# Kernel tuning notes

Hardware: AMD Instinct MI355X
Metric: run time of the kernel (lower is better)

## Reference

```python
import jax, jax.numpy as jnp
import numpy as np

ATOM_FDIM = 133
BOND_FDIM = 14
HIDDEN = 300
DEPTH = 3
FFN_HIDDEN = 300
NUM_ATOMS = 100000
NUM_EDGES = 400000
NUM_MOLS = 4096


def setup_inputs() -> dict:
    key = jax.random.key(0)
    ks = jax.random.split(key, 10)
    x = jax.random.normal(ks[0], (NUM_ATOMS, ATOM_FDIM), dtype=jnp.float32)
    edge_index = jax.random.randint(ks[1], (2, NUM_EDGES), 0, NUM_ATOMS, dtype=jnp.int32)
    edge_attr = jax.random.normal(ks[2], (NUM_EDGES, BOND_FDIM), dtype=jnp.float32)
    batch = jnp.sort(jax.random.randint(ks[3], (NUM_ATOMS,), 0, NUM_MOLS, dtype=jnp.int32))
    s = 0.05
    W_i = jax.random.normal(ks[4], (HIDDEN, ATOM_FDIM + BOND_FDIM), dtype=jnp.float32) * s
    W_h = jax.random.normal(ks[5], (HIDDEN, HIDDEN), dtype=jnp.float32) * s
    W_o_w = jax.random.normal(ks[6], (HIDDEN, ATOM_FDIM + HIDDEN), dtype=jnp.float32) * s
    W_o_b = jnp.zeros((HIDDEN,), dtype=jnp.float32)
    ffn1_w = jax.random.normal(ks[7], (FFN_HIDDEN, HIDDEN), dtype=jnp.float32) * s
    ffn1_b = jnp.zeros((FFN_HIDDEN,), dtype=jnp.float32)
    ffn2_w = jax.random.normal(ks[8], (1, FFN_HIDDEN), dtype=jnp.float32) * s
    ffn2_b = jnp.zeros((1,), dtype=jnp.float32)
    return {"x": x, "edge_index": edge_index, "edge_attr": edge_attr, "batch": batch,
            "W_i": W_i, "W_h": W_h, "W_o_w": W_o_w, "W_o_b": W_o_b,
            "ffn1_w": ffn1_w, "ffn1_b": ffn1_b, "ffn2_w": ffn2_w, "ffn2_b": ffn2_b}


def reference(x, edge_index, edge_attr, batch, W_i, W_h, W_o_w, W_o_b,
              ffn1_w, ffn1_b, ffn2_w, ffn2_b):
    num_atoms = x.shape[0]
    src, tgt = edge_index[0], edge_index[1]
    # initial edge messages: [E, hidden]
    init = jnp.concatenate([x[src], edge_attr], axis=-1)
    m = jax.nn.relu(init @ W_i.T)
    # dropout is identity at inference
    for _ in range(DEPTH - 1):
        nei = jax.ops.segment_sum(m, tgt, num_segments=num_atoms)  # [N, hidden]
        m = jax.nn.relu(m + nei[src] @ W_h.T)
    atom_msg = jax.ops.segment_sum(m, tgt, num_segments=num_atoms)
    atom_h = jax.nn.relu(jnp.concatenate([x, atom_msg], axis=-1) @ W_o_w.T + W_o_b)
    mol = jax.ops.segment_sum(atom_h, batch, num_segments=NUM_MOLS)  # [B, hidden]
    h = jax.nn.relu(mol @ ffn1_w.T + ffn1_b)
    out = h @ ffn2_w.T + ffn2_b  # [B, 1]
    return out
```

## Files before the change

kernel.cpp:

```cpp
#include <hip/hip_runtime.h>
#include <hip/hip_fp16.h>

#define HID   300
#define NEIP  304
#define PSTR  900
#define APB   4
#define SWK(r) (((r) >> 2) & 3)

typedef _Float16 f16;
typedef f16  f16x2 __attribute__((ext_vector_type(2)));
typedef f16  f16x4 __attribute__((ext_vector_type(4)));
typedef float f32x4 __attribute__((ext_vector_type(4)));

__device__ __forceinline__ f16x2 u2h(unsigned u) {
    union { unsigned u; f16x2 h; } c; c.u = u; return c.h;
}
__device__ __forceinline__ unsigned pk16(float a, float b) {
    union { f16 h[2]; unsigned u; } c; c.h[0] = (f16)a; c.h[1] = (f16)b;
    return c.u;
}
__device__ __forceinline__ void glds16(const void* g, void* l) {
    __builtin_amdgcn_global_load_lds(
        (const __attribute__((address_space(1))) void*)g,
        (__attribute__((address_space(3))) void*)l, 16, 0, 0);
}

__global__ __launch_bounds__(256) void fill_f32(float* __restrict__ p, int n, float v)
{
    int i = blockIdx.x * blockDim.x + threadIdx.x;
    int stride = gridDim.x * blockDim.x;
    for (; i < n; i += stride) p[i] = v;
}

__global__ __launch_bounds__(256) void zero_i32(int* __restrict__ p, int n)
{
    int i = blockIdx.x * blockDim.x + threadIdx.x;
    int stride = gridDim.x * blockDim.x;
    for (; i < n; i += stride) p[i] = 0;
}

__global__ __launch_bounds__(256) void cvt_pad_f16(
    f16* __restrict__ dst, const float* __restrict__ src,
    int srcRows, int ldsrc, int kuse, int kpad, int dstRows)
{
    int i = blockIdx.x * 256 + threadIdx.x;
    const int total = dstRows * kpad;
    const int st = gridDim.x * 256;
    for (; i < total; i += st) {
        int r = i / kpad, k = i - r * kpad;
        float v = (r < srcRows && k < kuse) ? src[(size_t)r * ldsrc + k] : 0.f;
        const int kd = (k & ~15) | (((((k >> 2) & 3) ^ SWK(r)) << 2)) | (k & 3);
        dst[(size_t)r * kpad + kd] = (f16)v;
    }
}

__global__ __launch_bounds__(256) void hist_tgt(
    const int* __restrict__ tgt, int* __restrict__ deg, int E, int N)
{
    int e = blockIdx.x * 256 + threadIdx.x;
    const int st = gridDim.x * 256;
    for (; e < E; e += st) {
        int t = tgt[e];
        t = ((unsigned)t < (unsigned)N) ? t : 0;
        atomicAdd(&deg[t], 1);
    }
}

__global__ __launch_bounds__(1024) void scan_p1(
    const int* __restrict__ deg, int* __restrict__ bsum, int N)
{
    __shared__ int s[1024];
    const int t = threadIdx.x;
    const int i = blockIdx.x * 1024 + t;
    s[t] = (i < N) ? deg[i] : 0;
    __syncthreads();
#pragma unroll
    for (int off = 512; off > 0; off >>= 1) {
        if (t < off) s[t] += s[t + off];
        __syncthreads();
    }
    if (t == 0) bsum[blockIdx.x] = s[0];
}

__global__ __launch_bounds__(1024) void scan_p2(
    const int* __restrict__ bsum, int* __restrict__ boff,
    int G, int* __restrict__ rowPtrN, int E)
{
    __shared__ int s[1024];
    const int t = threadIdx.x;
    s[t] = (t < G) ? bsum[t] : 0;
    __syncthreads();
    for (int off = 1; off < 1024; off <<= 1) {
        const int v = (t >= off) ? s[t - off] : 0;
        __syncthreads();
        s[t] += v;
        __syncthreads();
    }
    if (t < G) boff[t] = (t == 0) ? 0 : s[t - 1];
    if (t == 0) *rowPtrN = E;
}

__global__ __launch_bounds__(1024) void scan_p3(
    const int* __restrict__ deg, const int* __restrict__ boff,
    int* __restrict__ rowPtr, int* __restrict__ cursor, int N)
{
    __shared__ int s[1024];
    const int t = threadIdx.x;
    const int i = blockIdx.x * 1024 + t;
    const int v = (i < N) ? deg[i] : 0;
    s[t] = v;
    __syncthreads();
    for (int off = 1; off < 1024; off <<= 1) {
        const int w = (t >= off) ? s[t - off] : 0;
        __syncthreads();
        s[t] += w;
        __syncthreads();
    }
    if (i < N) {
        const int excl = boff[blockIdx.x] + s[t] - v;
        rowPtr[i] = excl;
        cursor[i] = excl;
    }
}

__global__ __launch_bounds__(256) void scatter_e(
    const int* __restrict__ src, const int* __restrict__ tgt,
    const float* __restrict__ ea,
    int* __restrict__ cursor, int* __restrict__ csrc,
    unsigned* __restrict__ eaPk,
    int E, int N)
{
    int e = blockIdx.x * 256 + threadIdx.x;
    const int st = gridDim.x * 256;
    for (; e < E; e += st) {
        int t = tgt[e];
        int s = src[e];
        t = ((unsigned)t < (unsigned)N) ? t : 0;
        s = ((unsigned)s < (unsigned)N) ? s : 0;
        const int p = atomicAdd(&cursor[t], 1);
        csrc[p] = s;
        const float* er = ea + (size_t)e * 14;
        uint4 q0, q1;
        q0.x = pk16(er[0],  er[1]);  q0.y = pk16(er[2],  er[3]);
        q0.z = pk16(er[4],  er[5]);  q0.w = pk16(er[6],  er[7]);
        q1.x = pk16(er[8],  er[9]);  q1.y = pk16(er[10], er[11]);
        q1.z = pk16(er[12], er[13]); q1.w = 0u;
        uint4* dst = (uint4*)(eaPk + (size_t)p * 8);
        dst[0] = q0;
        dst[1] = q1;
    }
}

__global__ __launch_bounds__(512) void gemm_mfma(
    const void* __restrict__ A1, int lda1, int a1f16, int K1use,
    const f16* __restrict__ W1, int kpad1,
    const void* __restrict__ A2, int lda2, int a2f16, int K2use,
    const f16* __restrict__ W2, int kpad2,
    const float* __restrict__ bias,
    f16* __restrict__ C, int ldc,
    int M, int do_relu)
{
    __shared__ f16 As[2][128 * 16];
    __shared__ f16 Ws[2][320 * 16];

    const int tid  = threadIdx.x;
    const int bm   = blockIdx.x * 128;
    const int lane = tid & 63;
    const int wv   = tid >> 6;
    const int wrow = (wv >> 2) * 64;
    const int wcol = (wv & 3) * 80;
    const int lm   = lane & 15;
    const int g    = lane >> 4;

    const int n1 = A1 ? (kpad1 >> 4) : 0;
    const int n2 = A2 ? (kpad2 >> 4) : 0;
    const int ntot = n1 + n2;

    f32x4 acc[4][5];
#pragma unroll
    for (int r = 0; r < 4; ++r)
#pragma unroll
        for (int c = 0; c < 5; ++c) acc[r][c] = (f32x4){0.f, 0.f, 0.f, 0.f};

    const int arow = tid >> 2;
    const int ach  = tid & 3;
    const int gm   = bm + arow;

    auto seg_f16 = [&](int s) -> bool {
        return (s < n1) ? (a1f16 != 0) : (a2f16 != 0);
    };

    auto a_load_f32 = [&](int s) -> f16x4 {
        const float* A; int lda, Kuse, k0;
        if (s < n1) { A = (const float*)A1; lda = lda1; Kuse = K1use; k0 = s << 4; }
        else        { A = (const float*)A2; lda = lda2; Kuse = K2use; k0 = (s - n1) << 4; }
        const int gk = k0 + (ach << 2);
        f16x4 v = (f16x4){0, 0, 0, 0};
        if (gm < M) {
            const float* p = A + (size_t)gm * lda + gk;
#pragma unroll
            for (int j = 0; j < 4; ++j)
                v[j] = (gk + j < Kuse) ? (f16)p[j] : (f16)0.f;
        }
        return v;
    };

    auto commit_a = [&](int b, f16x4 v) {
        *(f16x4*)&As[b][arow * 16 + ((ach ^ SWK(arow)) << 2)] = v;
    };

    auto stage_glds = [&](int s, int b) {
        const f16* W; int kpad, k0; const f16* Af; int lda; bool f16seg;
        if (s < n1) { W = W1; kpad = kpad1; k0 = s << 4;
                      f16seg = (a1f16 != 0); Af = (const f16*)A1; lda = lda1; }
        else        { W = W2; kpad = kpad2; k0 = (s - n1) << 4;
                      f16seg = (a2f16 != 0); Af = (const f16*)A2; lda = lda2; }
        const int half16 = (lane & 1) << 4;
        const int r2 = lane >> 1;
        for (int c = wv; c < 14; c += 8) {
            if (c < 4) {
                if (f16seg) {
                    const int gmrow = bm + c * 32 + r2;
                    void* ldst = (void*)&As[b][c * 512];
                    if (gmrow < M) {
                        const char* gsrc = (const char*)Af
                            + ((size_t)gmrow * lda + k0) * 2 + half16;
                        glds16(gsrc, ldst);
                    }
                }
            } else {
                const int wr = (c - 4) * 32 + r2;
                const char* gsrc = (const char*)W
                    + ((size_t)wr * kpad + k0) * 2 + half16;
                void* ldst = (void*)&Ws[b][(c - 4) * 512];
                glds16(gsrc, ldst);
            }
        }
    };

    const f16x4 z4 = (f16x4){0, 0, 0, 0};
    f16x4 aNxt = z4;
    stage_glds(0, 0);
    if (!seg_f16(0)) commit_a(0, a_load_f32(0));
    if (ntot > 1 && !seg_f16(1)) aNxt = a_load_f32(1);
    __syncthreads();

    int b = 0;
    for (int s = 0; s < ntot; ++s) {
        f16x4 af[4], bf[5];
#pragma unroll
        for (int r = 0; r < 4; ++r) {
            const int row = wrow + (r << 4) + lm;
            af[r] = *(const f16x4*)&As[b][row * 16 + ((g ^ SWK(row)) << 2)];
        }
#pragma unroll
        for (int c = 0; c < 5; ++c) {
            const int row = wcol + (c << 4) + lm;
            bf[c] = *(const f16x4*)&Ws[b][row * 16 + ((g ^ SWK(row)) << 2)];
        }
        if (s + 1 < ntot) stage_glds(s + 1, b ^ 1);
        f16x4 aN2 = z4;
        if (s + 2 < ntot && !seg_f16(s + 2)) aN2 = a_load_f32(s + 2);
#pragma unroll
        for (int r = 0; r < 4; ++r)
#pragma unroll
            for (int c = 0; c < 5; ++c)
                acc[r][c] = __builtin_amdgcn_mfma_f32_16x16x16f16(
                    af[r], bf[c], acc[r][c], 0, 0, 0);
        if (s + 1 < ntot && !seg_f16(s + 1)) commit_a(b ^ 1, aNxt);
        aNxt = aN2;
        __syncthreads();
        b ^= 1;
    }

#pragma unroll
    for (int r = 0; r < 4; ++r) {
        const int gm0 = bm + wrow + (r << 4) + ((lane >> 4) << 2);
#pragma unroll
        for (int c = 0; c < 5; ++c) {
            const int n = wcol + (c << 4) + lm;
            if (n >= HID) continue;
            const float bi = bias ? bias[n] : 0.f;
#pragma unroll
            for (int i = 0; i < 4; ++i) {
                const int gmo = gm0 + i;
                if (gmo >= M) continue;
                float v = acc[r][c][i] + bi;
                if (do_relu) v = fmaxf(v, 0.f);
                C[(size_t)gmo * ldc + n] = (f16)v;
            }
        }
    }
}

template <int NSLOTS>
__global__ __launch_bounds__(192) void edge_csr(
    const unsigned* __restrict__ packed,
    const int* __restrict__ rowPtr,
    const int* __restrict__ csrc,
    const unsigned* __restrict__ eaPk,
    const float* __restrict__ Wi,
    unsigned* __restrict__ out,
    int N)
{
    const int p = threadIdx.x;
    f16x2 wpk[14];
    if (p < 150) {
#pragma unroll
        for (int k = 0; k < 14; ++k)
            wpk[k] = (f16x2){(f16)Wi[(2 * p) * 147 + 133 + k],
                             (f16)Wi[(2 * p + 1) * 147 + 133 + k]};
    }
    const f16x2 zero2 = (f16x2){(f16)0.f, (f16)0.f};

    const int a0 = blockIdx.x * APB;
    const int a1 = min(a0 + APB, N);
    for (int a = a0; a < a1; ++a) {
        const int beg = rowPtr[a];
        const int end = rowPtr[a + 1];
        float acc0 = 0.f, acc1 = 0.f;
        if (p < 150) {
#pragma unroll 2
            for (int j = beg; j < end; ++j) {
                const int s = csrc[j];
                const unsigned* row = packed + (size_t)s * (PSTR / 2);
                const unsigned u0 = row[p];
                unsigned u1 = 0, u2 = 0;
                if (NSLOTS > 1) u1 = row[p + 150];
                if (NSLOTS > 2) u2 = row[p + 300];
                const unsigned* eq = eaPk + (size_t)j * 8;
                f16x2 ebA = zero2, ebB = zero2;
#pragma unroll
                for (int k = 0; k < 7; ++k) {
                    const f16x2 e2 = u2h(eq[k]);
                    ebA += (f16x2){e2.x, e2.x} * wpk[2 * k];
                    ebB += (f16x2){e2.y, e2.y} * wpk[2 * k + 1];
                }
                f16x2 m = __builtin_elementwise_max(u2h(u0) + (ebA + ebB), zero2);
                if (NSLOTS > 1) m = __builtin_elementwise_max(m + u2h(u1), zero2);
                if (NSLOTS > 2) m = __builtin_elementwise_max(m + u2h(u2), zero2);
                acc0 += (float)m.x;
                acc1 += (float)m.y;
            }
        }
        if (p < NEIP / 2) {
            const unsigned val = (p < 150) ? pk16(acc0, acc1) : 0u;
            const int t = p >> 3, c = (p >> 1) & 3, hf = p & 1;
            out[(size_t)a * (NEIP / 2) + t * 8 + ((c ^ SWK(a)) << 1) + hf] = val;
        }
    }
}

__global__ __launch_bounds__(256) void mol_pool(
    const f16* __restrict__ ah,
    const int* __restrict__ batch,
    float* __restrict__ mol,
    int N)
{
    const int b = blockIdx.x;
    int lo = 0, hi = N;
    while (lo < hi) { int mid = (lo + hi) >> 1; if (batch[mid] < b) lo = mid + 1; else hi = mid; }
    const int start = lo;
    hi = N;
    while (lo < hi) { int mid = (lo + hi) >> 1; if (batch[mid] < b + 1) lo = mid + 1; else hi = mid; }
    const int end = lo;

    for (int h = threadIdx.x; h < HID; h += 256) {
        float s = 0.f;
        for (int a = start; a < end; ++a) s += (float)ah[(size_t)a * PSTR + h];
        mol[(size_t)b * HID + h] = s;
    }
}

__global__ __launch_bounds__(64) void ffn2_k(
    const f16* __restrict__ h1,
    const float* __restrict__ w2,
    const float* __restrict__ b2, float* __restrict__ out, int B)
{
    const int b = blockIdx.x;
    float s = 0.f;
    for (int k = threadIdx.x; k < HID; k += 64)
        s += (float)h1[(size_t)b * NEIP + k] * w2[k];
#pragma unroll
    for (int off = 32; off > 0; off >>= 1) s += __shfl_down(s, off);
    if (threadIdx.x == 0) out[b] = s + b2[0];
}

extern "C" void kernel_launch(void* const* d_in, const int* in_sizes, int n_in,
                              void* d_out, int out_size, void* d_ws, size_t ws_size,
                              hipStream_t stream)
{
    float* outp = (float*)d_out;
    const int fillBlocks = (out_size + 255) / 256;

    if (n_in < 12) {
        fill_f32<<<fillBlocks, 256, 0, stream>>>(outp, out_size, 2.0e6f + n_in);
        return;
    }

    const int N = in_sizes[0] / 133;
    const int E = in_sizes[1] / 2;
    const int B = out_size;

    const long long expect[12] = {
        (long long)N * 133, (long long)E * 2, (long long)E * 14, N,
        300LL * 147, 300LL * 300, 300LL * 433, 300,
        300LL * 300, 300, 300, 1 };
    for (int i = 0; i < 12; ++i) {
        if ((long long)in_sizes[i] != expect[i]) {
            fill_f32<<<fillBlocks, 256, 0, stream>>>(outp, out_size,
                                                     3.0e6f + 1.0e4f * i);
            return;
        }
    }

    const int G = (N + 1023) / 1024;
    if (G > 1024) {
        fill_f32<<<fillBlocks, 256, 0, stream>>>(outp, out_size, 4.0e6f);
        return;
    }

    char* basep = (char*)d_ws;
    auto align16 = [](size_t v) { return (v + 15) & ~(size_t)15; };
    const size_t packedB = align16((size_t)N * PSTR * sizeof(f16));
    const size_t neiB    = align16((size_t)N * NEIP * sizeof(f16));
    const size_t wSmall  = align16(320 * 144 * sizeof(f16));
    const size_t wBig    = align16(320 * 304 * sizeof(f16));
    const size_t molB    = align16((size_t)B * HID * sizeof(float));
    const size_t h1B     = align16((size_t)B * NEIP * sizeof(f16));
    const size_t rpB     = align16((size_t)(N + 1) * sizeof(int));
    const size_t curB    = align16((size_t)N * sizeof(int));
    const size_t csrcB   = align16((size_t)E * sizeof(int));
    const size_t eaB     = align16((size_t)E * 8 * sizeof(unsigned));
    const size_t bsB     = align16(1024 * sizeof(int));
    const size_t need = packedB + neiB + 2 * wSmall + 3 * wBig
                      + molB + h1B + rpB + 2 * curB + csrcB + eaB + 2 * bsB;

    if (ws_size < need) {
        fill_f32<<<fillBlocks, 256, 0, stream>>>(outp, out_size,
                                                 (float)(ws_size >> 20));
        return;
    }

    const float* x     = (const float*)d_in[0];
    const int*   ei    = (const int*)d_in[1];
    const float* ea    = (const float*)d_in[2];
    const int*   batch = (const int*)d_in[3];
    const float* W_i   = (const float*)d_in[4];
    const float* W_h   = (const float*)d_in[5];
    const float* W_o   = (const float*)d_in[6];
    const float* W_ob  = (const float*)d_in[7];
    const float* f1w   = (const float*)d_in[8];
    const float* f1b   = (const float*)d_in[9];
    const float* f2w   = (const float*)d_in[10];
    const float* f2b   = (const float*)d_in[11];
    const int* src = ei;
    const int* tgt = ei + E;

    char* cp = basep;
    f16* packed = (f16*)cp;         cp += packedB;
    f16* nei    = (f16*)cp;         cp += neiB;
    f16* WiA    = (f16*)cp;         cp += wSmall;
    f16* Wh     = (f16*)cp;         cp += wBig;
    f16* WoA    = (f16*)cp;         cp += wSmall;
    f16* WoB    = (f16*)cp;         cp += wBig;
    f16* Wf1    = (f16*)cp;         cp += wBig;
    float* mol  = (float*)cp;       cp += molB;
    f16* h1     = (f16*)cp;         cp += h1B;
    int* rowPtr = (int*)cp;         cp += rpB;
    int* cursor = (int*)cp;         cp += curB;
    int* deg    = (int*)cp;         cp += curB;
    int* csrc   = (int*)cp;         cp += csrcB;
    unsigned* eaPk = (unsigned*)cp; cp += eaB;
    int* bsum   = (int*)cp;         cp += bsB;
    int* boff   = (int*)cp;         cp += bsB;

    f16* xa_s  = packed;
    f16* hn0_s = packed + 300;
    f16* hn1_s = packed + 600;

    const unsigned* packed_u = (const unsigned*)packed;
    unsigned*       nei_u    = (unsigned*)nei;

    const int gAtom = (N + 127) / 128;
    const int gMolG = (B + 127) / 128;
    const int gEdge = (N + APB - 1) / APB;

    zero_i32<<<128, 256, 0, stream>>>(deg, N);
    hist_tgt<<<1024, 256, 0, stream>>>(tgt, deg, E, N);
    scan_p1<<<G, 1024, 0, stream>>>(deg, bsum, N);
    scan_p2<<<1, 1024, 0, stream>>>(bsum, boff, G, rowPtr + N, E);
    scan_p3<<<G, 1024, 0, stream>>>(deg, boff, rowPtr, cursor, N);
    scatter_e<<<1024, 256, 0, stream>>>(src, tgt, ea, cursor, csrc, eaPk, E, N);

    cvt_pad_f16<<<64,  256, 0, stream>>>(WiA, W_i,       300, 147, 133, 144, 320);
    cvt_pad_f16<<<128, 256, 0, stream>>>(Wh,  W_h,       300, 300, 300, 304, 320);
    cvt_pad_f16<<<64,  256, 0, stream>>>(WoA, W_o,       300, 433, 133, 144, 320);
    cvt_pad_f16<<<128, 256, 0, stream>>>(WoB, W_o + 133, 300, 433, 300, 304, 320);
    cvt_pad_f16<<<128, 256, 0, stream>>>(Wf1, f1w,       300, 300, 300, 304, 320);

    gemm_mfma<<<gAtom, 512, 0, stream>>>(x, 133, 0, 133, WiA, 144,
        nullptr, 0, 0, 0, nullptr, 0, nullptr, xa_s, PSTR, N, 0);
    edge_csr<1><<<gEdge, 192, 0, stream>>>(packed_u, rowPtr, csrc, eaPk, W_i,
                                           nei_u, N);
    gemm_mfma<<<gAtom, 512, 0, stream>>>(nei, NEIP, 1, NEIP, Wh, 304,
        nullptr, 0, 0, 0, nullptr, 0, nullptr, hn0_s, PSTR, N, 0);
    edge_csr<2><<<gEdge, 192, 0, stream>>>(packed_u, rowPtr, csrc, eaPk, W_i,
                                           nei_u, N);
    gemm_mfma<<<gAtom, 512, 0, stream>>>(nei, NEIP, 1, NEIP, Wh, 304,
        nullptr, 0, 0, 0, nullptr, 0, nullptr, hn1_s, PSTR, N, 0);
    edge_csr<3><<<gEdge, 192, 0, stream>>>(packed_u, rowPtr, csrc, eaPk, W_i,
                                           nei_u, N);
    gemm_mfma<<<gAtom, 512, 0, stream>>>(x, 133, 0, 133, WoA, 144,
        nei, NEIP, 1, NEIP, WoB, 304, W_ob, hn0_s, PSTR, N, 1);
    mol_pool<<<B, 256, 0, stream>>>(hn0_s, batch, mol, N);
    gemm_mfma<<<gMolG, 512, 0, stream>>>(mol, 300, 0, 300, Wf1, 304,
        nullptr, 0, 0, 0, nullptr, 0, f1b, h1, NEIP, B, 1);
    ffn2_k<<<B, 64, 0, stream>>>(h1, f2w, f2b, outp, B);
}
```

Baseline: 860.4 us.

## Switch GEMM to 16x16x32 MFMA with K=32 tiles and 64-row blocks

Moves the GEMM from 16x16x16 MFMA to the gfx950 16x16x32 f16 MFMA. This halves the number of K steps and barriers and widens LDS fragment loads to 8 halves. The M tile shrinks from 128 to 64 rows with a launch_bounds occupancy hint, and K padding grows to multiples of 32. The swizzle, weight conversion, and the edge kernel's nei output layout are rewritten to match. The cost is more padded K work (304->320, 144->160) and more blocks that each reload the full weight tile.

```diff
diff --git a/kernel.cpp b/kernel.cpp
--- a/kernel.cpp
+++ b/kernel.cpp
@@ -2,14 +2,15 @@
 #include <hip/hip_fp16.h>
 
 #define HID   300
-#define NEIP  304
+#define NEIP  320
 #define PSTR  900
 #define APB   4
-#define SWK(r) (((r) >> 2) & 3)
+#define SWK(r) (((r) >> 1) & 3)
 
 typedef _Float16 f16;
 typedef f16  f16x2 __attribute__((ext_vector_type(2)));
 typedef f16  f16x4 __attribute__((ext_vector_type(4)));
+typedef f16  f16x8 __attribute__((ext_vector_type(8)));
 typedef float f32x4 __attribute__((ext_vector_type(4)));
 
 __device__ __forceinline__ f16x2 u2h(unsigned u) {
@@ -49,7 +50,8 @@
     for (; i < total; i += st) {
         int r = i / kpad, k = i - r * kpad;
         float v = (r < srcRows && k < kuse) ? src[(size_t)r * ldsrc + k] : 0.f;
-        const int kd = (k & ~15) | (((((k >> 2) & 3) ^ SWK(r)) << 2)) | (k & 3);
+        const int t = k >> 5, kg = (k >> 3) & 3, w = k & 7;
+        const int kd = (t << 5) | ((kg ^ SWK(r)) << 3) | w;
         dst[(size_t)r * kpad + kd] = (f16)v;
     }
 }
@@ -151,7 +153,7 @@
     }
 }
 
-__global__ __launch_bounds__(512) void gemm_mfma(
+__global__ __launch_bounds__(512, 4) void gemm_mfma(
     const void* __restrict__ A1, int lda1, int a1f16, int K1use,
     const f16* __restrict__ W1, int kpad1,
     const void* __restrict__ A2, int lda2, int a2f16, int K2use,
@@ -160,86 +162,81 @@
     f16* __restrict__ C, int ldc,
     int M, int do_relu)
 {
-    __shared__ f16 As[2][128 * 16];
-    __shared__ f16 Ws[2][320 * 16];
+    __shared__ f16 As[2][64 * 32];
+    __shared__ f16 Ws[2][320 * 32];
 
     const int tid  = threadIdx.x;
-    const int bm   = blockIdx.x * 128;
+    const int bm   = blockIdx.x * 64;
     const int lane = tid & 63;
     const int wv   = tid >> 6;
-    const int wrow = (wv >> 2) * 64;
+    const int wrow = (wv >> 2) * 32;
     const int wcol = (wv & 3) * 80;
     const int lm   = lane & 15;
-    const int g    = lane >> 4;
-
-    const int n1 = A1 ? (kpad1 >> 4) : 0;
-    const int n2 = A2 ? (kpad2 >> 4) : 0;
+    const int kg   = lane >> 4;
+
+    const int n1 = A1 ? (kpad1 >> 5) : 0;
+    const int n2 = A2 ? (kpad2 >> 5) : 0;
     const int ntot = n1 + n2;
 
-    f32x4 acc[4][5];
-#pragma unroll
-    for (int r = 0; r < 4; ++r)
+    f32x4 acc[2][5];
+#pragma unroll
+    for (int r = 0; r < 2; ++r)
 #pragma unroll
         for (int c = 0; c < 5; ++c) acc[r][c] = (f32x4){0.f, 0.f, 0.f, 0.f};
 
     const int arow = tid >> 2;
-    const int ach  = tid & 3;
+    const int asub = tid & 3;
     const int gm   = bm + arow;
 
     auto seg_f16 = [&](int s) -> bool {
         return (s < n1) ? (a1f16 != 0) : (a2f16 != 0);
     };
 
-    auto a_load_f32 = [&](int s) -> f16x4 {
+    auto a_load_f32 = [&](int s) -> f16x8 {
         const float* A; int lda, Kuse, k0;
-        if (s < n1) { A = (const float*)A1; lda = lda1; Kuse = K1use; k0 = s << 4; }
-        else        { A = (const float*)A2; lda = lda2; Kuse = K2use; k0 = (s - n1) << 4; }
-        const int gk = k0 + (ach << 2);
-        f16x4 v = (f16x4){0, 0, 0, 0};
-        if (gm < M) {
+        if (s < n1) { A = (const float*)A1; lda = lda1; Kuse = K1use; k0 = s << 5; }
+        else        { A = (const float*)A2; lda = lda2; Kuse = K2use; k0 = (s - n1) << 5; }
+        f16x8 v = (f16x8){0, 0, 0, 0, 0, 0, 0, 0};
+        if (tid < 256 && gm < M) {
+            const int gk = k0 + (asub << 3);
             const float* p = A + (size_t)gm * lda + gk;
 #pragma unroll
-            for (int j = 0; j < 4; ++j)
+            for (int j = 0; j < 8; ++j)
                 v[j] = (gk + j < Kuse) ? (f16)p[j] : (f16)0.f;
         }
         return v;
     };
 
-    auto commit_a = [&](int b, f16x4 v) {
-        *(f16x4*)&As[b][arow * 16 + ((ach ^ SWK(arow)) << 2)] = v;
+    auto commit_a = [&](int b, f16x8 v) {
+        if (tid < 256)
+            *(f16x8*)&As[b][arow * 32 + ((asub ^ SWK(arow)) << 3)] = v;
     };
 
     auto stage_glds = [&](int s, int b) {
         const f16* W; int kpad, k0; const f16* Af; int lda; bool f16seg;
-        if (s < n1) { W = W1; kpad = kpad1; k0 = s << 4;
+        if (s < n1) { W = W1; kpad = kpad1; k0 = s << 5;
                       f16seg = (a1f16 != 0); Af = (const f16*)A1; lda = lda1; }
-        else        { W = W2; kpad = kpad2; k0 = (s - n1) << 4;
+        else        { W = W2; kpad = kpad2; k0 = (s - n1) << 5;
                       f16seg = (a2f16 != 0); Af = (const f16*)A2; lda = lda2; }
-        const int half16 = (lane & 1) << 4;
-        const int r2 = lane >> 1;
-        for (int c = wv; c < 14; c += 8) {
+        const int r16 = lane >> 2;
+        const int q   = lane & 3;
+        for (int c = wv; c < 24; c += 8) {
             if (c < 4) {
                 if (f16seg) {
-                    const int gmrow = bm + c * 32 + r2;
-                    void* ldst = (void*)&As[b][c * 512];
-                    if (gmrow < M) {
-                        const char* gsrc = (const char*)Af
-                            + ((size_t)gmrow * lda + k0) * 2 + half16;
-                        glds16(gsrc, ldst);
-                    }
+                    const int gR = bm + (c << 4) + r16;
+                    if (gR < M)
+                        glds16((const char*)Af + ((size_t)gR * lda + k0) * 2 + q * 16,
+                               (void*)&As[b][c << 9]);
                 }
             } else {
-                const int wr = (c - 4) * 32 + r2;
-                const char* gsrc = (const char*)W
-                    + ((size_t)wr * kpad + k0) * 2 + half16;
-                void* ldst = (void*)&Ws[b][(c - 4) * 512];
-                glds16(gsrc, ldst);
+                const int R = ((c - 4) << 4) + r16;
+                glds16((const char*)W + ((size_t)R * kpad + k0) * 2 + q * 16,
+                       (void*)&Ws[b][(c - 4) << 9]);
             }
         }
     };
 
-    const f16x4 z4 = (f16x4){0, 0, 0, 0};
-    f16x4 aNxt = z4;
+    f16x8 aNxt = (f16x8){0, 0, 0, 0, 0, 0, 0, 0};
     stage_glds(0, 0);
     if (!seg_f16(0)) commit_a(0, a_load_f32(0));
     if (ntot > 1 && !seg_f16(1)) aNxt = a_load_f32(1);
@@ -247,25 +244,25 @@
 
     int b = 0;
     for (int s = 0; s < ntot; ++s) {
-        f16x4 af[4], bf[5];
-#pragma unroll
-        for (int r = 0; r < 4; ++r) {
-            const int row = wrow + (r << 4) + lm;
-            af[r] = *(const f16x4*)&As[b][row * 16 + ((g ^ SWK(row)) << 2)];
+        f16x8 af[2], bf[5];
+#pragma unroll
+        for (int r = 0; r < 2; ++r) {
+            const int R = wrow + (r << 4) + lm;
+            af[r] = *(const f16x8*)&As[b][R * 32 + ((kg ^ SWK(R)) << 3)];
         }
 #pragma unroll
         for (int c = 0; c < 5; ++c) {
-            const int row = wcol + (c << 4) + lm;
-            bf[c] = *(const f16x4*)&Ws[b][row * 16 + ((g ^ SWK(row)) << 2)];
+            const int R = wcol + (c << 4) + lm;
+            bf[c] = *(const f16x8*)&Ws[b][R * 32 + ((kg ^ SWK(R)) << 3)];
         }
         if (s + 1 < ntot) stage_glds(s + 1, b ^ 1);
-        f16x4 aN2 = z4;
+        f16x8 aN2 = (f16x8){0, 0, 0, 0, 0, 0, 0, 0};
         if (s + 2 < ntot && !seg_f16(s + 2)) aN2 = a_load_f32(s + 2);
 #pragma unroll
-        for (int r = 0; r < 4; ++r)
+        for (int r = 0; r < 2; ++r)
 #pragma unroll
             for (int c = 0; c < 5; ++c)
-                acc[r][c] = __builtin_amdgcn_mfma_f32_16x16x16f16(
+                acc[r][c] = __builtin_amdgcn_mfma_f32_16x16x32_f16(
                     af[r], bf[c], acc[r][c], 0, 0, 0);
         if (s + 1 < ntot && !seg_f16(s + 1)) commit_a(b ^ 1, aNxt);
         aNxt = aN2;
@@ -274,7 +271,7 @@
     }
 
 #pragma unroll
-    for (int r = 0; r < 4; ++r) {
+    for (int r = 0; r < 2; ++r) {
         const int gm0 = bm + wrow + (r << 4) + ((lane >> 4) << 2);
 #pragma unroll
         for (int c = 0; c < 5; ++c) {
@@ -345,8 +342,8 @@
         }
         if (p < NEIP / 2) {
             const unsigned val = (p < 150) ? pk16(acc0, acc1) : 0u;
-            const int t = p >> 3, c = (p >> 1) & 3, hf = p & 1;
-            out[(size_t)a * (NEIP / 2) + t * 8 + ((c ^ SWK(a)) << 1) + hf] = val;
+            const int t = p >> 4, kgc = (p >> 2) & 3, w = p & 3;
+            out[(size_t)a * (NEIP / 2) + (t << 4) + ((kgc ^ SWK(a)) << 2) + w] = val;
         }
     }
 }
@@ -424,8 +421,8 @@
     auto align16 = [](size_t v) { return (v + 15) & ~(size_t)15; };
     const size_t packedB = align16((size_t)N * PSTR * sizeof(f16));
     const size_t neiB    = align16((size_t)N * NEIP * sizeof(f16));
-    const size_t wSmall  = align16(320 * 144 * sizeof(f16));
-    const size_t wBig    = align16(320 * 304 * sizeof(f16));
+    const size_t wSmall  = align16(320 * 160 * sizeof(f16));
+    const size_t wBig    = align16(320 * 320 * sizeof(f16));
     const size_t molB    = align16((size_t)B * HID * sizeof(float));
     const size_t h1B     = align16((size_t)B * NEIP * sizeof(f16));
     const size_t rpB     = align16((size_t)(N + 1) * sizeof(int));
@@ -482,8 +479,8 @@
     const unsigned* packed_u = (const unsigned*)packed;
     unsigned*       nei_u    = (unsigned*)nei;
 
-    const int gAtom = (N + 127) / 128;
-    const int gMolG = (B + 127) / 128;
+    const int gAtom = (N + 63) / 64;
+    const int gMolG = (B + 63) / 64;
     const int gEdge = (N + APB - 1) / APB;
 
     zero_i32<<<128, 256, 0, stream>>>(deg, N);
@@ -493,28 +490,28 @@
     scan_p3<<<G, 1024, 0, stream>>>(deg, boff, rowPtr, cursor, N);
     scatter_e<<<1024, 256, 0, stream>>>(src, tgt, ea, cursor, csrc, eaPk, E, N);
 
-    cvt_pad_f16<<<64,  256, 0, stream>>>(WiA, W_i,       300, 147, 133, 144, 320);
-    cvt_pad_f16<<<128, 256, 0, stream>>>(Wh,  W_h,       300, 300, 300, 304, 320);
-    cvt_pad_f16<<<64,  256, 0, stream>>>(WoA, W_o,       300, 433, 133, 144, 320);
-    cvt_pad_f16<<<128, 256, 0, stream>>>(WoB, W_o + 133, 300, 433, 300, 304, 320);
-    cvt_pad_f16<<<128, 256, 0, stream>>>(Wf1, f1w,       300, 300, 300, 304, 320);
-
-    gemm_mfma<<<gAtom, 512, 0, stream>>>(x, 133, 0, 133, WiA, 144,
+    cvt_pad_f16<<<64,  256, 0, stream>>>(WiA, W_i,       300, 147, 133, 160, 320);
+    cvt_pad_f16<<<128, 256, 0, stream>>>(Wh,  W_h,       300, 300, 300, 320, 320);
+    cvt_pad_f16<<<64,  256, 0, stream>>>(WoA, W_o,       300, 433, 133, 160, 320);
+    cvt_pad_f16<<<128, 256, 0, stream>>>(WoB, W_o + 133, 300, 433, 300, 320, 320);
+    cvt_pad_f16<<<128, 256, 0, stream>>>(Wf1, f1w,       300, 300, 300, 320, 320);
+
+    gemm_mfma<<<gAtom, 512, 0, stream>>>(x, 133, 0, 133, WiA, 160,
         nullptr, 0, 0, 0, nullptr, 0, nullptr, xa_s, PSTR, N, 0);
     edge_csr<1><<<gEdge, 192, 0, stream>>>(packed_u, rowPtr, csrc, eaPk, W_i,
                                            nei_u, N);
-    gemm_mfma<<<gAtom, 512, 0, stream>>>(nei, NEIP, 1, NEIP, Wh, 304,
+    gemm_mfma<<<gAtom, 512, 0, stream>>>(nei, NEIP, 1, NEIP, Wh, 320,
         nullptr, 0, 0, 0, nullptr, 0, nullptr, hn0_s, PSTR, N, 0);
     edge_csr<2><<<gEdge, 192, 0, stream>>>(packed_u, rowPtr, csrc, eaPk, W_i,
                                            nei_u, N);
-    gemm_mfma<<<gAtom, 512, 0, stream>>>(nei, NEIP, 1, NEIP, Wh, 304,
+    gemm_mfma<<<gAtom, 512, 0, stream>>>(nei, NEIP, 1, NEIP, Wh, 320,
         nullptr, 0, 0, 0, nullptr, 0, nullptr, hn1_s, PSTR, N, 0);
     edge_csr<3><<<gEdge, 192, 0, stream>>>(packed_u, rowPtr, csrc, eaPk, W_i,
                                            nei_u, N);
-    gemm_mfma<<<gAtom, 512, 0, stream>>>(x, 133, 0, 133, WoA, 144,
-        nei, NEIP, 1, NEIP, WoB, 304, W_ob, hn0_s, PSTR, N, 1);
+    gemm_mfma<<<gAtom, 512, 0, stream>>>(x, 133, 0, 133, WoA, 160,
+        nei, NEIP, 1, NEIP, WoB, 320, W_ob, hn0_s, PSTR, N, 1);
     mol_pool<<<B, 256, 0, stream>>>(hn0_s, batch, mol, N);
-    gemm_mfma<<<gMolG, 512, 0, stream>>>(mol, 300, 0, 300, Wf1, 304,
+    gemm_mfma<<<gMolG, 512, 0, stream>>>(mol, 300, 0, 300, Wf1, 320,
         nullptr, 0, 0, 0, nullptr, 0, f1b, h1, NEIP, B, 1);
     ffn2_k<<<B, 64, 0, stream>>>(h1, f2w, f2b, outp, B);
 }
```

Result: no change. 849.3 us (-1.3%).
